# Optimization experiments

Hardware: AMD Instinct MI355X
Metric: run time of the kernel (lower is better)

The kernel has to match this reference:

```python
import jax, jax.numpy as jnp
import numpy as np
import math

A = 32; B = 32; PSIZE = 16; K = 3; STRIDE = 2; PAD = 1; ITERS = 3; FINAL_LAMBDA = 0.01
KK = K * K; KKA = KK * A; KKA2 = KKA // 2 + 1
EPS = 1e-12; LN2PI = math.log(2 * math.pi)


def unfold(x, k, s, p):
    # torch F.unfold: output feature dim ordered (C, kh, kw), columns row-major
    b, C, h, w = x.shape
    xp = jnp.pad(x, ((0, 0), (0, 0), (p, p), (p, p)))
    oh = (h + 2 * p - k) // s + 1
    ow = (w + 2 * p - k) // s + 1
    cols = [xp[:, :, ki:ki + s * (oh - 1) + 1:s, kj:kj + s * (ow - 1) + 1:s]
            for ki in range(k) for kj in range(k)]
    patches = jnp.stack(cols, axis=2)  # [b, C, kk, oh, ow]
    return patches.reshape(b, C, k * k, oh * ow), oh, ow


def setup_inputs():
    key = jax.random.key(0)
    ks = jax.random.split(key, 8)
    b, h, w = 4, 14, 14
    a_in = jax.random.uniform(ks[0], (b, A, h, w), dtype=jnp.float32)
    pose = jax.random.normal(ks[1], (b, A * PSIZE, h, w), dtype=jnp.float32)
    mpose_w = jax.random.normal(ks[2], (B * PSIZE, PSIZE), dtype=jnp.float32) / np.float32(np.sqrt(PSIZE))
    mpose_b = jnp.zeros((B * PSIZE,), jnp.float32)
    freq_w = jax.random.normal(ks[3], (KKA2, PSIZE, 2), dtype=jnp.float32) * 0.02
    ln_g = jnp.ones((A,), jnp.float32)
    ln_b = jnp.zeros((A,), jnp.float32)
    lim = np.float32(np.sqrt(6.0 / (KK + KK)))  # xavier_uniform on [kk, kk, 1]
    spat_w = jax.random.uniform(ks[4], (KK, KK, 1), jnp.float32, -lim, lim)
    spat_bias = jnp.ones((KK,), jnp.float32)
    beta_u = jnp.zeros((1, 1, B, 1), jnp.float32)
    beta_a = jnp.zeros((1, 1, B), jnp.float32)
    return dict(a_in=a_in, pose=pose, mpose_w=mpose_w, mpose_b=mpose_b,
                freq_w=freq_w, ln_g=ln_g, ln_b=ln_b, spat_w=spat_w,
                spat_bias=spat_bias, beta_u=beta_u, beta_a=beta_a)


def _forward(a_in, pose, mpose_w, mpose_b, freq_w, ln_g, ln_b,
             spat_w, spat_bias, beta_u, beta_a):
    b = a_in.shape[0]
    pose_u, oh, ow = unfold(pose, K, STRIDE, PAD)  # [b, A*PSIZE, KK, l]
    l = oh * ow
    pose_u = pose_u.reshape(b, A, PSIZE, KK, l)
    pose_u = pose_u.transpose(0, 4, 3, 1, 2).reshape(b, l, KKA, PSIZE)
    # mpose linear: psize -> B*psize
    po = jnp.einsum('blkp,qp->blkq', pose_u, mpose_w) + mpose_b
    po = po.reshape(b * l, KKA, B, PSIZE)
    # Frequency FFT filter over kkA axis (weight shared across all B slices)
    xf = jnp.fft.rfft(po, axis=1, norm='ortho')        # [bl, KKA2, B, PSIZE] complex
    wc = freq_w[..., 0] + 1j * freq_w[..., 1]           # [KKA2, PSIZE]
    xf = xf * wc[None, :, None, :]
    po = jnp.fft.irfft(xf, n=KKA, axis=1, norm='ortho') + po  # residual
    v = po.reshape(b, l, KKA, B, PSIZE)
    a_u, _, _ = unfold(a_in, K, STRIDE, PAD)            # [b, A, KK, l]
    a_u = a_u.transpose(0, 3, 2, 1).reshape(b, l, KKA)
    # Spatial gating applied to ones-initialized r (identical for every B slice)
    ones = jnp.ones((b * l, KKA), jnp.float32)
    g = ones.reshape(b * l, KK, A)
    mu_g = g.mean(-1, keepdims=True)
    var_g = ((g - mu_g) ** 2).mean(-1, keepdims=True)
    gn = (g - mu_g) / jnp.sqrt(var_g + 1e-5) * ln_g + ln_b
    g2 = jnp.einsum('ij,nja->nia', spat_w[:, :, 0], gn) + spat_bias[None, :, None]
    gate = jax.nn.gelu(g2, approximate=False).reshape(b * l, KKA) + ones
    logit = jnp.broadcast_to(gate[:, :, None], (b * l, KKA, B))
    r = jax.nn.softmax(logit, axis=2).reshape(b, l, KKA, B, 1)
    a_out = mu = None
    for i in range(ITERS):
        lam = FINAL_LAMBDA * (1.0 - 0.95 ** (i + 1))
        # m-step
        rr = r * a_u[:, :, :, None, None]
        r_sum = rr.sum(axis=2, keepdims=True)                 # [b,l,1,B,1]
        coeff = rr / (r_sum + EPS)
        mu = (coeff * v).sum(axis=2, keepdims=True)           # [b,l,1,B,PSIZE]
        sig = (coeff * (v - mu) ** 2).sum(axis=2, keepdims=True) + EPS
        cost = (beta_u + jnp.log(jnp.sqrt(sig[:, :, 0]))) * r_sum[:, :, 0]  # [b,l,B,PSIZE]
        a_out = jax.nn.sigmoid(lam * (beta_a - cost.sum(axis=3)))           # [b,l,B]
        if i < ITERS - 1:
            # e-step (note: log(sigma_sq * ln2pi) is faithful to the original code)
            ln_p = (-0.5 * jnp.sum(jnp.log(sig * LN2PI), axis=-1)
                    - jnp.sum((v - mu) ** 2 / (2.0 * sig), axis=-1))        # [b,l,KKA,B]
            ln_ap = ln_p + jnp.log(a_out[:, :, None, :])
            r = jax.nn.softmax(ln_ap, axis=-1)[..., None]
    pose_out = mu[:, :, 0].reshape(b, l, B * PSIZE).transpose(0, 2, 1).reshape(b, B * PSIZE, oh, ow)
    a_fin = a_out.transpose(0, 2, 1).reshape(b, B, oh, ow)
    return a_fin, pose_out


def reference(a_in, pose, mpose_w, mpose_b, freq_w, ln_g, ln_b,
              spat_w, spat_bias, beta_u, beta_a):
    return _forward(a_in, pose, mpose_w, mpose_b, freq_w, ln_g, ln_b,
                    spat_w, spat_bias, beta_u, beta_a)
```

## Files before the change

### kernel.cpp

```cpp
#include <hip/hip_runtime.h>
#include <hip/hip_bf16.h>
#include <math.h>

#define A_    32
#define B_    32
#define PS    16
#define KK_   9
#define KKA_  288
#define OH_   7
#define L_    49
#define NB    4
#define NSITE 196
#define NCOLS 3136

#define LAM1 5.0e-4f
#define LAM2 9.75e-4f
#define LAM3 1.42625e-3f
#define LOG_LN2PI 0.6086775903077413f

typedef _Float16 half2v __attribute__((ext_vector_type(2)));
typedef short    short8 __attribute__((ext_vector_type(8)));
typedef float    floatx4 __attribute__((ext_vector_type(4)));

static __device__ __forceinline__ float san(float x, float lo, float hi){
    return fminf(fmaxf(x, lo), hi);
}

static __device__ __forceinline__ float dot2acc(half2v a, half2v b, float c){
#if __has_builtin(__builtin_amdgcn_fdot2)
    return __builtin_amdgcn_fdot2(a, b, c, false);
#else
    return c + (float)a.x*(float)b.x + (float)a.y*(float)b.y;
#endif
}

__global__ void k_prep(const float* __restrict__ fw, const float* __restrict__ pose,
                       ushort* __restrict__ cpr, float* __restrict__ csum,
                       __hip_bfloat16* __restrict__ Xt, int nc)
{
    if ((int)blockIdx.x < nc){
        int id = (int)blockIdx.x*256 + threadIdx.x;
        if (id >= 16*288) return;
        int p = id / 288, m = id % 288;
        float acc = fw[(0*16 + p)*2 + 0];
        for (int k = 1; k <= 143; ++k){
            float re = fw[(k*16 + p)*2 + 0];
            float im = fw[(k*16 + p)*2 + 1];
            int km = (k*m) % 288;
            float ang = 0.021816615649929116f * (float)km;
            float s, c; __sincosf(ang, &s, &c);
            acc += 2.0f*(re*c - im*s);
        }
        float re144 = fw[(144*16 + p)*2 + 0];
        acc += re144 * ((m & 1) ? -1.0f : 1.0f);
        float cv = acc * (1.0f/288.0f);
        if (m == 0) cv += 1.0f;
        cv = san(cv, -1e4f, 1e4f);

        __hip_bfloat16 hb = __float2bfloat16(cv);
        float hif = __bfloat162float(hb);
        __hip_bfloat16 lb = __float2bfloat16(cv - hif);
        ushort hi = *(ushort*)&hb, lo = *(ushort*)&lb;

        ushort* c0h = cpr + p*592;
        ushort* c1h = cpr + 16*592   + p*592;
        ushort* c0l = cpr + 16*592*2 + p*592;
        ushort* c1l = cpr + 16*592*3 + p*592;
        int x1 = 288 - m;
        c0h[x1] = hi;  c0l[x1] = lo;
        c1h[x1-1] = hi; c1l[x1-1] = lo;
        if (m >= 1){
            int x2 = 576 - m;
            c0h[x2] = hi;  c0l[x2] = lo;
            c1h[x2-1] = hi; c1l[x2-1] = lo;
        } else {
            c0h[0] = hi; c0l[0] = lo;
            csum[p] = san(1.0f + fw[(0*16 + p)*2 + 0], -1e4f, 1e4f);
        }
        return;
    }
    int id = ((int)blockIdx.x - nc)*256 + threadIdx.x;
    if (id >= NCOLS*KKA_/8) return;
    int c = id / (KKA_/8), j8 = id % (KKA_/8);
    int j = j8*8;
    int n = c >> 4, q = c & 15;
    int bs = n / L_, l = n % L_, oy = l / OH_, ox = l % OH_;
    int kk = j >> 5, a0 = j & 31;
    int y = oy*2 - 1 + kk/3, x = ox*2 - 1 + kk%3;
    const bool inb = ((unsigned)y < 14u && (unsigned)x < 14u);
    const float* psrc = pose + (((long)bs*(A_*PS))*14 + y)*14 + x;
    union { ushort us[8]; uint4 u4; } res;
    #pragma unroll
    for (int u = 0; u < 8; ++u){
        float v = 0.f;
        if (inb) v = psrc[((a0+u)*PS + q)*196];
        __hip_bfloat16 hb = __float2bfloat16(san(v, -1e4f, 1e4f));
        res.us[u] = *(ushort*)&hb;
    }
    *(uint4*)&Xt[c*KKA_ + j] = res.u4;
}

__launch_bounds__(512, 1)
__global__ void
k_mega(const ushort* __restrict__ cpr, const __hip_bfloat16* __restrict__ Xt,
       const float* __restrict__ a_in,
       const float* __restrict__ mpw, const float* __restrict__ mpb,
       const float* __restrict__ csum,
       const float* __restrict__ beta_u, const float* __restrict__ beta_a,
       float* __restrict__ out)
{
    const int nl = blockIdx.x;
    const int t = threadIdx.x;
    const int Bc = t >> 4, p = t & 15;
    const int bs = nl / L_, l = nl % L_;

    __shared__ uint v_lds[56][512];
    __shared__ __align__(16) float scratch[9792];
    __shared__ float a_s[KKA_];
    __shared__ float cst[32];

    float* const dall = scratch;

    for (int j = t; j < KKA_; j += 512){
        int kk = j >> 5, a = j & 31;
        int oy = l / OH_, ox = l % OH_;
        int y = oy*2 - 1 + kk/3, x = ox*2 - 1 + kk%3;
        float v = 0.f;
        if ((unsigned)y < 14u && (unsigned)x < 14u)
            v = a_in[((bs*A_ + a)*14 + y)*14 + x];
        a_s[j] = san(v, 0.f, 1e4f);
    }
    half2v w_h[8];
    #pragma unroll
    for (int k = 0; k < 8; ++k){
        w_h[k].x = (_Float16)mpw[t*16 + 2*k];
        w_h[k].y = (_Float16)mpw[t*16 + 2*k + 1];
    }
    const float vb = mpb[t] * csum[p];
    const float bu = beta_u[Bc];
    const float ba = beta_a[Bc];

    const int w = t >> 6, lane = t & 63;
    const int mn = lane & 15, quad = lane >> 4;
    const int p0 = w*2;

    short8 bf[9];
    {
        const __hip_bfloat16* xrow = Xt + (nl*16 + mn)*KKA_ + quad*8;
        #pragma unroll
        for (int k = 0; k < 9; ++k) bf[k] = *(const short8*)&xrow[k*32];
    }
    __syncthreads();

    float s0a = 0.f, s0b = 0.f, s0c = 0.f, s0d = 0.f;
    for (int j = 0; j < KKA_; j += 4){
        s0a += a_s[j]; s0b += a_s[j+1]; s0c += a_s[j+2]; s0d += a_s[j+3];
    }
    const float S0tot = (s0a + s0b) + (s0c + s0d);

    float S1 = 0.f, S2 = 0.f;
    half2v v_h[88];

    auto do_chunk = [&](int ch, _Float16* usb){
        floatx4 accA = {0,0,0,0}, accB = {0,0,0,0};
        #pragma unroll
        for (int k0i = 0; k0i < 9; ++k0i){
            const int k0 = k0i*32;
            short8 bfrag = bf[k0i];
            #pragma unroll
            for (int pp = 0; pp < 2; ++pp){
                const int pg = p0 + pp;
                int o = 288 + k0 + quad*8 - (ch*16 + mn);
                int sel = o & 1, off = o - sel;
                const ushort* bh = cpr + (sel ? 16*592 : 0) + pg*592;
                const ushort* bl = cpr + 16*592*2 + (sel ? 16*592 : 0) + pg*592;
                short8 ah = *(const short8*)&bh[off];
                short8 al = *(const short8*)&bl[off];
                floatx4 acc = pp ? accB : accA;
                acc = __builtin_amdgcn_mfma_f32_16x16x32_bf16(ah, bfrag, acc, 0, 0, 0);
                acc = __builtin_amdgcn_mfma_f32_16x16x32_bf16(al, bfrag, acc, 0, 0, 0);
                if (pp) accB = acc; else accA = acc;
            }
        }
        #pragma unroll
        for (int r = 0; r < 4; ++r){
            usb[p0*264     + (quad*4 + r)*16 + mn] = (_Float16)accA[r];
            usb[(p0+1)*264 + (quad*4 + r)*16 + mn] = (_Float16)accB[r];
        }
    };

    auto vpair = [&](const _Float16* urow, int s, float& v0o, float& v1o){
        union { uint4 u4; half2v h2[4]; } A0, A1, B0, B1;
        A0.u4 = *(const uint4*)&urow[(2*s)*16];
        A1.u4 = *(const uint4*)&urow[(2*s)*16 + 8];
        B0.u4 = *(const uint4*)&urow[(2*s+1)*16];
        B1.u4 = *(const uint4*)&urow[(2*s+1)*16 + 8];
        float v0 = vb, v1 = vb;
        #pragma unroll
        for (int m = 0; m < 4; ++m){
            v0 = dot2acc(A0.h2[m], w_h[m],   v0);
            v0 = dot2acc(A1.h2[m], w_h[4+m], v0);
            v1 = dot2acc(B0.h2[m], w_h[m],   v1);
            v1 = dot2acc(B1.h2[m], w_h[4+m], v1);
        }
        v0o = v0; v1o = v1;
    };

    for (int ch = 0; ch < 7; ++ch){
        _Float16* usb = ((_Float16*)scratch) + (ch & 1)*4224;
        do_chunk(ch, usb);
        __syncthreads();
        const _Float16* urow = &usb[p*264];
        #pragma unroll
        for (int s = 0; s < 8; ++s){
            float v0, v1; vpair(urow, s, v0, v1);
            const int i0 = ch*16 + 2*s;
            const float a0 = a_s[i0], a1 = a_s[i0+1];
            S1 += a0*v0 + a1*v1;
            S2 += a0*v0*v0 + a1*v1*v1;
            union { half2v h; uint u; } cv;
            cv.h.x = (_Float16)v0; cv.h.y = (_Float16)v1;
            v_lds[ch*8 + s][t] = cv.u;
        }
    }
    #pragma unroll
    for (int c2 = 0; c2 < 11; ++c2){
        const int ch = 7 + c2;
        _Float16* usb = ((_Float16*)scratch) + (ch & 1)*4224;
        do_chunk(ch, usb);
        __syncthreads();
        const _Float16* urow = &usb[p*264];
        #pragma unroll
        for (int s = 0; s < 8; ++s){
            float v0, v1; vpair(urow, s, v0, v1);
            const int i0 = ch*16 + 2*s;
            const float a0 = a_s[i0], a1 = a_s[i0+1];
            S1 += a0*v0 + a1*v1;
            S2 += a0*v0*v0 + a1*v1*v1;
            half2v vh; vh.x = (_Float16)v0; vh.y = (_Float16)v1;
            v_h[c2*8 + s] = vh;
        }
    }

    float mu_r, i2s_r;
    {
        const float rs  = S0tot * (1.0f/32.0f);
        const float inv = 1.0f / (rs + 1e-12f);
        const float S1r = S1 * (1.0f/32.0f), S2r = S2 * (1.0f/32.0f);
        mu_r = S1r * inv;
        const float sg  = fmaxf((S2r - 2.f*mu_r*S1r + mu_r*mu_r*rs) * inv, 0.f) + 1e-12f;
        i2s_r = 0.5f / sg;
        const float lg  = logf(sg);
        float cs = (bu + 0.5f*lg) * rs;
        float ls = lg + LOG_LN2PI;
        #pragma unroll
        for (int m = 1; m < 16; m <<= 1){ cs += __shfl_xor(cs, m, 16); ls += __shfl_xor(ls, m, 16); }
        const float aout = san(1.f/(1.f + expf(-LAM1*(ba - cs))), 1e-30f, 1.f);
        if (p == 0) cst[Bc] = logf(aout) - 0.5f*ls;
    }
    __syncthreads();

    const int b0 = p & 1, b1 = (p>>1)&1, b2 = (p>>2)&1, b3 = (p>>3)&1;
    const int isub = t >> 5, Bce = t & 31;
    float muF = 0.f, aF = 0.f;
    for (int it = 0; it < 2; ++it){
        const float lam = it ? LAM3 : LAM2;

        auto dtree = [&](int ibase, auto getpair){
            float e1[8], e2[4], e3[2], dfin;
            #pragma unroll
            for (int s = 0; s < 8; ++s){
                float v0, v1; getpair(s, v0, v1);
                float d0 = v0 - mu_r, d1 = v1 - mu_r;
                float ea = d0*d0*i2s_r, eb = d1*d1*i2s_r;
                float aown  = b0 ? eb : ea;
                float asend = b0 ? ea : eb;
                e1[s] = aown + __shfl_xor(asend, 1);
            }
            #pragma unroll
            for (int s = 0; s < 4; ++s){
                float aown  = b1 ? e1[2*s+1] : e1[2*s];
                float asend = b1 ? e1[2*s]   : e1[2*s+1];
                e2[s] = aown + __shfl_xor(asend, 2);
            }
            #pragma unroll
            for (int s = 0; s < 2; ++s){
                float aown  = b2 ? e2[2*s+1] : e2[2*s];
                float asend = b2 ? e2[2*s]   : e2[2*s+1];
                e3[s] = aown + __shfl_xor(asend, 4);
            }
            {
                float aown  = b3 ? e3[1] : e3[0];
                float asend = b3 ? e3[0] : e3[1];
                dfin = aown + __shfl_xor(asend, 8);
            }
            dall[(ibase + p)*34 + Bc] = dfin;
        };
        #pragma unroll
        for (int g = 0; g < 7; ++g)
            dtree(g*16, [&](int s, float& v0, float& v1){
                union { uint u; half2v h; } cv; cv.u = v_lds[g*8 + s][t];
                v0 = (float)cv.h.x; v1 = (float)cv.h.y; });
        #pragma unroll
        for (int c2 = 0; c2 < 11; ++c2)
            dtree((7+c2)*16, [&](int s, float& v0, float& v1){
                half2v vh = v_h[c2*8 + s];
                v0 = (float)vh.x; v1 = (float)vh.y; });
        __syncthreads();

        {
            const float cb = cst[Bce];
            #pragma unroll
            for (int g = 0; g < 18; ++g){
                float* dp = &dall[(g*16 + isub)*34 + Bce];
                float lnap = cb - *dp;
                float mx = lnap;
                #pragma unroll
                for (int m = 16; m >= 1; m >>= 1) mx = fmaxf(mx, __shfl_xor(mx, m));
                float ex = expf(lnap - mx);
                float sm = ex;
                #pragma unroll
                for (int m = 16; m >= 1; m >>= 1) sm += __shfl_xor(sm, m);
                *dp = (ex / sm) * a_s[g*16 + isub];
            }
        }
        __syncthreads();

        float T0 = 0.f, T1 = 0.f, T2 = 0.f;
        auto csum3 = [&](int ibase, auto getpair){
            #pragma unroll
            for (int s = 0; s < 8; ++s){
                float v0, v1; getpair(s, v0, v1);
                float r0 = dall[(ibase + 2*s)*34 + Bc];
                float r1 = dall[(ibase + 2*s + 1)*34 + Bc];
                T0 += r0 + r1;
                T1 += r0*v0 + r1*v1;
                T2 += r0*v0*v0 + r1*v1*v1;
            }
        };
        #pragma unroll
        for (int g = 0; g < 7; ++g)
            csum3(g*16, [&](int s, float& v0, float& v1){
                union { uint u; half2v h; } cv; cv.u = v_lds[g*8 + s][t];
                v0 = (float)cv.h.x; v1 = (float)cv.h.y; });
        #pragma unroll
        for (int c2 = 0; c2 < 11; ++c2)
            csum3((7+c2)*16, [&](int s, float& v0, float& v1){
                half2v vh = v_h[c2*8 + s];
                v0 = (float)vh.x; v1 = (float)vh.y; });

        const float inv = 1.f/(T0 + 1e-12f);
        const float mu  = T1 * inv;
        const float sg  = fmaxf((T2 - 2.f*mu*T1 + mu*mu*T0) * inv, 0.f) + 1e-12f;
        const float lg  = logf(sg);
        float cs = (bu + 0.5f*lg) * T0;
        float ls = lg + LOG_LN2PI;
        #pragma unroll
        for (int m = 1; m < 16; m <<= 1){ cs += __shfl_xor(cs, m, 16); ls += __shfl_xor(ls, m, 16); }
        const float aout = san(1.f/(1.f + expf(-lam*(ba - cs))), 1e-30f, 1.f);
        if (it == 0){
            mu_r = mu; i2s_r = 0.5f/sg;
            if (p == 0) cst[Bc] = logf(aout) - 0.5f*ls;
            __syncthreads();
        } else { muF = mu; aF = aout; }
    }

    if (p == 0) out[bs*(B_*L_) + Bc*L_ + l] = san(aF, 0.f, 1.f);
    out[6272 + (bs*512 + t)*L_ + l] = san(muF, -1e4f, 1e4f);
}

extern "C" void kernel_launch(void* const* d_in, const int* in_sizes, int n_in,
                              void* d_out, int out_size, void* d_ws, size_t ws_size,
                              hipStream_t stream)
{
    const float* a_in   = (const float*)d_in[0];
    const float* pose   = (const float*)d_in[1];
    const float* mpw    = (const float*)d_in[2];
    const float* mpb    = (const float*)d_in[3];
    const float* fw     = (const float*)d_in[4];
    const float* beta_u = (const float*)d_in[9];
    const float* beta_a = (const float*)d_in[10];
    float* out = (float*)d_out;

    char* base = (char*)d_ws;
    float*  csum = (float*)(base + 0);
    ushort* cpr  = (ushort*)(base + 256);
    __hip_bfloat16* Xt = (__hip_bfloat16*)(base + 76288);

    const int nc = 18;
    const int nx = (NCOLS*KKA_/8 + 255)/256;
    k_prep<<<nc + nx, 256, 0, stream>>>(fw, pose, cpr, csum, Xt, nc);
    k_mega<<<NSITE, 512, 0, stream>>>(cpr, Xt, a_in, mpw, mpb, csum, beta_u, beta_a, out);
}
```

Before: 258.0 us.

## Rebalance vote storage across LDS, registers and recompute to allow two blocks per CU

The kernel now lets the compiler target up to two waves per EU, and shrinks per-block storage to fit. The LDS vote buffer drops from 56 to 48 rows, the register vote array from 88 to 80 entries, and the B-fragment registers are re-read from global memory on each chunk instead of being held. The last two chunks are no longer stored; their votes are recomputed from the retained fp16 transform buffers in each routing pass. The aim is higher occupancy to hide latency, at the cost of extra global loads, repeated dot products, and possible register spills.

```diff
diff --git a/kernel.cpp b/kernel.cpp
--- a/kernel.cpp
+++ b/kernel.cpp
@@ -100,8 +100,8 @@
     *(uint4*)&Xt[c*KKA_ + j] = res.u4;
 }
 
-__launch_bounds__(512, 1)
-__global__ void
+__global__ __attribute__((amdgpu_flat_work_group_size(512,512), amdgpu_waves_per_eu(1,2)))
+void
 k_mega(const ushort* __restrict__ cpr, const __hip_bfloat16* __restrict__ Xt,
        const float* __restrict__ a_in,
        const float* __restrict__ mpw, const float* __restrict__ mpb,
@@ -114,12 +114,11 @@
     const int Bc = t >> 4, p = t & 15;
     const int bs = nl / L_, l = nl % L_;
 
-    __shared__ uint v_lds[56][512];
-    __shared__ __align__(16) float scratch[9792];
+    __shared__ uint v_lds[48][512];
+    __shared__ __align__(16) _Float16 us[2*4224];
+    __shared__ float dall[288*34];
     __shared__ float a_s[KKA_];
     __shared__ float cst[32];
-
-    float* const dall = scratch;
 
     for (int j = t; j < KKA_; j += 512){
         int kk = j >> 5, a = j & 31;
@@ -139,34 +138,27 @@
     const float vb = mpb[t] * csum[p];
     const float bu = beta_u[Bc];
     const float ba = beta_a[Bc];
+    __syncthreads();
+
+    float s0a = 0.f, s0b = 0.f, s0c = 0.f, s0d = 0.f;
+    for (int j = 0; j < KKA_; j += 4){
+        s0a += a_s[j]; s0b += a_s[j+1]; s0c += a_s[j+2]; s0d += a_s[j+3];
+    }
+    const float S0tot = (s0a + s0b) + (s0c + s0d);
 
     const int w = t >> 6, lane = t & 63;
     const int mn = lane & 15, quad = lane >> 4;
     const int p0 = w*2;
-
-    short8 bf[9];
-    {
-        const __hip_bfloat16* xrow = Xt + (nl*16 + mn)*KKA_ + quad*8;
-        #pragma unroll
-        for (int k = 0; k < 9; ++k) bf[k] = *(const short8*)&xrow[k*32];
-    }
-    __syncthreads();
-
-    float s0a = 0.f, s0b = 0.f, s0c = 0.f, s0d = 0.f;
-    for (int j = 0; j < KKA_; j += 4){
-        s0a += a_s[j]; s0b += a_s[j+1]; s0c += a_s[j+2]; s0d += a_s[j+3];
-    }
-    const float S0tot = (s0a + s0b) + (s0c + s0d);
+    const __hip_bfloat16* xrow = Xt + (nl*16 + mn)*KKA_ + quad*8;
 
     float S1 = 0.f, S2 = 0.f;
-    half2v v_h[88];
+    half2v v_h[80];
 
     auto do_chunk = [&](int ch, _Float16* usb){
         floatx4 accA = {0,0,0,0}, accB = {0,0,0,0};
-        #pragma unroll
         for (int k0i = 0; k0i < 9; ++k0i){
             const int k0 = k0i*32;
-            short8 bfrag = bf[k0i];
+            short8 bfrag = *(const short8*)&xrow[k0];
             #pragma unroll
             for (int pp = 0; pp < 2; ++pp){
                 const int pg = p0 + pp;
@@ -206,8 +198,8 @@
         v0o = v0; v1o = v1;
     };
 
-    for (int ch = 0; ch < 7; ++ch){
-        _Float16* usb = ((_Float16*)scratch) + (ch & 1)*4224;
+    for (int ch = 0; ch < 6; ++ch){
+        _Float16* usb = us + (ch & 1)*4224;
         do_chunk(ch, usb);
         __syncthreads();
         const _Float16* urow = &usb[p*264];
@@ -224,9 +216,9 @@
         }
     }
     #pragma unroll
-    for (int c2 = 0; c2 < 11; ++c2){
-        const int ch = 7 + c2;
-        _Float16* usb = ((_Float16*)scratch) + (ch & 1)*4224;
+    for (int c2 = 0; c2 < 10; ++c2){
+        const int ch = 6 + c2;
+        _Float16* usb = us + (ch & 1)*4224;
         do_chunk(ch, usb);
         __syncthreads();
         const _Float16* urow = &usb[p*264];
@@ -239,6 +231,21 @@
             S2 += a0*v0*v0 + a1*v1*v1;
             half2v vh; vh.x = (_Float16)v0; vh.y = (_Float16)v1;
             v_h[c2*8 + s] = vh;
+        }
+    }
+    #pragma unroll
+    for (int ch = 16; ch < 18; ++ch){
+        _Float16* usb = us + (ch & 1)*4224;
+        do_chunk(ch, usb);
+        __syncthreads();
+        const _Float16* urow = &usb[p*264];
+        #pragma unroll
+        for (int s = 0; s < 8; ++s){
+            float v0, v1; vpair(urow, s, v0, v1);
+            const int i0 = ch*16 + 2*s;
+            const float a0 = a_s[i0], a1 = a_s[i0+1];
+            S1 += a0*v0 + a1*v1;
+            S2 += a0*v0*v0 + a1*v1*v1;
         }
     }
 
@@ -296,16 +303,21 @@
             }
             dall[(ibase + p)*34 + Bc] = dfin;
         };
-        #pragma unroll
-        for (int g = 0; g < 7; ++g)
+        for (int g = 0; g < 6; ++g)
             dtree(g*16, [&](int s, float& v0, float& v1){
                 union { uint u; half2v h; } cv; cv.u = v_lds[g*8 + s][t];
                 v0 = (float)cv.h.x; v1 = (float)cv.h.y; });
         #pragma unroll
-        for (int c2 = 0; c2 < 11; ++c2)
-            dtree((7+c2)*16, [&](int s, float& v0, float& v1){
+        for (int c2 = 0; c2 < 10; ++c2)
+            dtree((6+c2)*16, [&](int s, float& v0, float& v1){
                 half2v vh = v_h[c2*8 + s];
                 v0 = (float)vh.x; v1 = (float)vh.y; });
+        #pragma unroll
+        for (int ch = 16; ch < 18; ++ch){
+            const _Float16* urow = &us[(ch & 1)*4224 + p*264];
+            dtree(ch*16, [&](int s, float& v0, float& v1){
+                vpair(urow, s, v0, v1); });
+        }
         __syncthreads();
 
         {
@@ -338,16 +350,21 @@
                 T2 += r0*v0*v0 + r1*v1*v1;
             }
         };
-        #pragma unroll
-        for (int g = 0; g < 7; ++g)
+        for (int g = 0; g < 6; ++g)
             csum3(g*16, [&](int s, float& v0, float& v1){
                 union { uint u; half2v h; } cv; cv.u = v_lds[g*8 + s][t];
                 v0 = (float)cv.h.x; v1 = (float)cv.h.y; });
         #pragma unroll
-        for (int c2 = 0; c2 < 11; ++c2)
-            csum3((7+c2)*16, [&](int s, float& v0, float& v1){
+        for (int c2 = 0; c2 < 10; ++c2)
+            csum3((6+c2)*16, [&](int s, float& v0, float& v1){
                 half2v vh = v_h[c2*8 + s];
                 v0 = (float)vh.x; v1 = (float)vh.y; });
+        #pragma unroll
+        for (int ch = 16; ch < 18; ++ch){
+            const _Float16* urow = &us[(ch & 1)*4224 + p*264];
+            csum3(ch*16, [&](int s, float& v0, float& v1){
+                vpair(urow, s, v0, v1); });
+        }
 
         const float inv = 1.f/(T0 + 1e-12f);
         const float mu  = T1 * inv;
```

Measured after the change: 257.2 us. No clear change (-0.3%).

## Rebalance vote storage across LDS, registers and retained MFMA chunks

Applied to the files above, without the earlier changes.

Vote storage is redistributed. Six chunks now go to LDS (down from seven) and nine to registers (down from eleven). The last three chunks keep their raw MFMA outputs in a triple-buffered LDS region and are recomputed from there with vpair during the E-steps instead of being stored. The B-fragment registers are dropped, so Xt is reloaded from global memory in each k step, and several loops are left without unroll pragmas. The dall stride also changes from 34 to 33, which alters the LDS bank pattern. The aim is lower register pressure without extra LDS, at the cost of recomputing the dot products and more global loads.

```diff
diff --git a/kernel.cpp b/kernel.cpp
--- a/kernel.cpp
+++ b/kernel.cpp
@@ -17,6 +17,8 @@
 #define LAM2 9.75e-4f
 #define LAM3 1.42625e-3f
 #define LOG_LN2PI 0.6086775903077413f
+
+#define DSTR 33
 
 typedef _Float16 half2v __attribute__((ext_vector_type(2)));
 typedef short    short8 __attribute__((ext_vector_type(8)));
@@ -114,12 +116,11 @@
     const int Bc = t >> 4, p = t & 15;
     const int bs = nl / L_, l = nl % L_;
 
-    __shared__ uint v_lds[56][512];
-    __shared__ __align__(16) float scratch[9792];
+    __shared__ uint v_lds[48][512];
+    __shared__ __align__(16) _Float16 us[3*4224];
+    __shared__ float dall[288*DSTR];
     __shared__ float a_s[KKA_];
     __shared__ float cst[32];
-
-    float* const dall = scratch;
 
     for (int j = t; j < KKA_; j += 512){
         int kk = j >> 5, a = j & 31;
@@ -139,34 +140,27 @@
     const float vb = mpb[t] * csum[p];
     const float bu = beta_u[Bc];
     const float ba = beta_a[Bc];
+    __syncthreads();
+
+    float s0a = 0.f, s0b = 0.f, s0c = 0.f, s0d = 0.f;
+    for (int j = 0; j < KKA_; j += 4){
+        s0a += a_s[j]; s0b += a_s[j+1]; s0c += a_s[j+2]; s0d += a_s[j+3];
+    }
+    const float S0tot = (s0a + s0b) + (s0c + s0d);
 
     const int w = t >> 6, lane = t & 63;
     const int mn = lane & 15, quad = lane >> 4;
     const int p0 = w*2;
-
-    short8 bf[9];
-    {
-        const __hip_bfloat16* xrow = Xt + (nl*16 + mn)*KKA_ + quad*8;
-        #pragma unroll
-        for (int k = 0; k < 9; ++k) bf[k] = *(const short8*)&xrow[k*32];
-    }
-    __syncthreads();
-
-    float s0a = 0.f, s0b = 0.f, s0c = 0.f, s0d = 0.f;
-    for (int j = 0; j < KKA_; j += 4){
-        s0a += a_s[j]; s0b += a_s[j+1]; s0c += a_s[j+2]; s0d += a_s[j+3];
-    }
-    const float S0tot = (s0a + s0b) + (s0c + s0d);
+    const __hip_bfloat16* xrow = Xt + (nl*16 + mn)*KKA_ + quad*8;
 
     float S1 = 0.f, S2 = 0.f;
-    half2v v_h[88];
+    half2v v_h[72];
 
     auto do_chunk = [&](int ch, _Float16* usb){
         floatx4 accA = {0,0,0,0}, accB = {0,0,0,0};
-        #pragma unroll
         for (int k0i = 0; k0i < 9; ++k0i){
             const int k0 = k0i*32;
-            short8 bfrag = bf[k0i];
+            short8 bfrag = *(const short8*)&xrow[k0];
             #pragma unroll
             for (int pp = 0; pp < 2; ++pp){
                 const int pg = p0 + pp;
@@ -206,8 +200,8 @@
         v0o = v0; v1o = v1;
     };
 
-    for (int ch = 0; ch < 7; ++ch){
-        _Float16* usb = ((_Float16*)scratch) + (ch & 1)*4224;
+    for (int ch = 0; ch < 6; ++ch){
+        _Float16* usb = us + (ch % 3)*4224;
         do_chunk(ch, usb);
         __syncthreads();
         const _Float16* urow = &usb[p*264];
@@ -223,24 +217,39 @@
             v_lds[ch*8 + s][t] = cv.u;
         }
     }
-    #pragma unroll
-    for (int c2 = 0; c2 < 11; ++c2){
-        const int ch = 7 + c2;
-        _Float16* usb = ((_Float16*)scratch) + (ch & 1)*4224;
-        do_chunk(ch, usb);
-        __syncthreads();
-        const _Float16* urow = &usb[p*264];
-        #pragma unroll
-        for (int s = 0; s < 8; ++s){
-            float v0, v1; vpair(urow, s, v0, v1);
-            const int i0 = ch*16 + 2*s;
-            const float a0 = a_s[i0], a1 = a_s[i0+1];
-            S1 += a0*v0 + a1*v1;
-            S2 += a0*v0*v0 + a1*v1*v1;
-            half2v vh; vh.x = (_Float16)v0; vh.y = (_Float16)v1;
-            v_h[c2*8 + s] = vh;
-        }
-    }
+
+#define P1_REG(C2) { \
+        _Float16* usb = us + ((6+(C2)) % 3)*4224; \
+        do_chunk(6+(C2), usb); \
+        __syncthreads(); \
+        const _Float16* urow = &usb[p*264]; \
+        _Pragma("unroll") \
+        for (int s = 0; s < 8; ++s){ \
+            float v0, v1; vpair(urow, s, v0, v1); \
+            const int i0 = (6+(C2))*16 + 2*s; \
+            const float a0 = a_s[i0], a1 = a_s[i0+1]; \
+            S1 += a0*v0 + a1*v1; \
+            S2 += a0*v0*v0 + a1*v1*v1; \
+            half2v vh; vh.x = (_Float16)v0; vh.y = (_Float16)v1; \
+            v_h[(C2)*8 + s] = vh; } }
+    P1_REG(0) P1_REG(1) P1_REG(2) P1_REG(3) P1_REG(4)
+    P1_REG(5) P1_REG(6) P1_REG(7) P1_REG(8)
+#undef P1_REG
+
+#define P1_RET(CH) { \
+        _Float16* usb = us + ((CH) % 3)*4224; \
+        do_chunk((CH), usb); \
+        __syncthreads(); \
+        const _Float16* urow = &usb[p*264]; \
+        _Pragma("unroll") \
+        for (int s = 0; s < 8; ++s){ \
+            float v0, v1; vpair(urow, s, v0, v1); \
+            const int i0 = (CH)*16 + 2*s; \
+            const float a0 = a_s[i0], a1 = a_s[i0+1]; \
+            S1 += a0*v0 + a1*v1; \
+            S2 += a0*v0*v0 + a1*v1*v1; } }
+    P1_RET(15) P1_RET(16) P1_RET(17)
+#undef P1_RET
 
     float mu_r, i2s_r;
     {
@@ -294,25 +303,30 @@
                 float asend = b3 ? e3[0] : e3[1];
                 dfin = aown + __shfl_xor(asend, 8);
             }
-            dall[(ibase + p)*34 + Bc] = dfin;
+            dall[(ibase + p)*DSTR + Bc] = dfin;
         };
-        #pragma unroll
-        for (int g = 0; g < 7; ++g)
+        for (int g = 0; g < 6; ++g)
             dtree(g*16, [&](int s, float& v0, float& v1){
                 union { uint u; half2v h; } cv; cv.u = v_lds[g*8 + s][t];
                 v0 = (float)cv.h.x; v1 = (float)cv.h.y; });
-        #pragma unroll
-        for (int c2 = 0; c2 < 11; ++c2)
-            dtree((7+c2)*16, [&](int s, float& v0, float& v1){
-                half2v vh = v_h[c2*8 + s];
-                v0 = (float)vh.x; v1 = (float)vh.y; });
+#define DT_REG(C2) dtree((6+(C2))*16, [&](int s, float& v0, float& v1){ \
+            half2v vh = v_h[(C2)*8 + s]; v0 = (float)vh.x; v1 = (float)vh.y; });
+        DT_REG(0) DT_REG(1) DT_REG(2) DT_REG(3) DT_REG(4)
+        DT_REG(5) DT_REG(6) DT_REG(7) DT_REG(8)
+#undef DT_REG
+        { const _Float16* ur = &us[0*4224 + p*264];
+          dtree(15*16, [&](int s, float& v0, float& v1){ vpair(ur, s, v0, v1); }); }
+        { const _Float16* ur = &us[1*4224 + p*264];
+          dtree(16*16, [&](int s, float& v0, float& v1){ vpair(ur, s, v0, v1); }); }
+        { const _Float16* ur = &us[2*4224 + p*264];
+          dtree(17*16, [&](int s, float& v0, float& v1){ vpair(ur, s, v0, v1); }); }
         __syncthreads();
 
         {
             const float cb = cst[Bce];
             #pragma unroll
             for (int g = 0; g < 18; ++g){
-                float* dp = &dall[(g*16 + isub)*34 + Bce];
+                float* dp = &dall[(g*16 + isub)*DSTR + Bce];
                 float lnap = cb - *dp;
                 float mx = lnap;
                 #pragma unroll
@@ -331,23 +345,28 @@
             #pragma unroll
             for (int s = 0; s < 8; ++s){
                 float v0, v1; getpair(s, v0, v1);
-                float r0 = dall[(ibase + 2*s)*34 + Bc];
-                float r1 = dall[(ibase + 2*s + 1)*34 + Bc];
+                float r0 = dall[(ibase + 2*s)*DSTR + Bc];
+                float r1 = dall[(ibase + 2*s + 1)*DSTR + Bc];
                 T0 += r0 + r1;
                 T1 += r0*v0 + r1*v1;
                 T2 += r0*v0*v0 + r1*v1*v1;
             }
         };
-        #pragma unroll
-        for (int g = 0; g < 7; ++g)
+        for (int g = 0; g < 6; ++g)
             csum3(g*16, [&](int s, float& v0, float& v1){
                 union { uint u; half2v h; } cv; cv.u = v_lds[g*8 + s][t];
                 v0 = (float)cv.h.x; v1 = (float)cv.h.y; });
-        #pragma unroll
-        for (int c2 = 0; c2 < 11; ++c2)
-            csum3((7+c2)*16, [&](int s, float& v0, float& v1){
-                half2v vh = v_h[c2*8 + s];
-                v0 = (float)vh.x; v1 = (float)vh.y; });
+#define CS_REG(C2) csum3((6+(C2))*16, [&](int s, float& v0, float& v1){ \
+            half2v vh = v_h[(C2)*8 + s]; v0 = (float)vh.x; v1 = (float)vh.y; });
+        CS_REG(0) CS_REG(1) CS_REG(2) CS_REG(3) CS_REG(4)
+        CS_REG(5) CS_REG(6) CS_REG(7) CS_REG(8)
+#undef CS_REG
+        { const _Float16* ur = &us[0*4224 + p*264];
+          csum3(15*16, [&](int s, float& v0, float& v1){ vpair(ur, s, v0, v1); }); }
+        { const _Float16* ur = &us[1*4224 + p*264];
+          csum3(16*16, [&](int s, float& v0, float& v1){ vpair(ur, s, v0, v1); }); }
+        { const _Float16* ur = &us[2*4224 + p*264];
+          csum3(17*16, [&](int s, float& v0, float& v1){ vpair(ur, s, v0, v1); }); }
 
         const float inv = 1.f/(T0 + 1e-12f);
         const float mu  = T1 * inv;
```

Measured after the change: 259.9 us. No clear change (+0.7%).

## Spill vote tensor to global scratch instead of LDS and registers

Applied to the files above, without the earlier changes.

The per-site vote matrix v was previously split between a large LDS array and 88 half2 registers per thread. It now lives entirely in a global workspace buffer that is written once and re-read in each EM iteration. The B fragments are reloaded from global per chunk instead of being held in registers, and the dall stride changes from 34 to 33. This frees LDS and registers, but it adds global memory round-trips, relying on L2 to keep them cheap.

```diff
diff --git a/kernel.cpp b/kernel.cpp
--- a/kernel.cpp
+++ b/kernel.cpp
@@ -17,6 +17,8 @@
 #define LAM2 9.75e-4f
 #define LAM3 1.42625e-3f
 #define LOG_LN2PI 0.6086775903077413f
+
+#define DSTR 33
 
 typedef _Float16 half2v __attribute__((ext_vector_type(2)));
 typedef short    short8 __attribute__((ext_vector_type(8)));
@@ -107,6 +109,7 @@
        const float* __restrict__ mpw, const float* __restrict__ mpb,
        const float* __restrict__ csum,
        const float* __restrict__ beta_u, const float* __restrict__ beta_a,
+       uint* __restrict__ vg,
        float* __restrict__ out)
 {
     const int nl = blockIdx.x;
@@ -114,12 +117,12 @@
     const int Bc = t >> 4, p = t & 15;
     const int bs = nl / L_, l = nl % L_;
 
-    __shared__ uint v_lds[56][512];
-    __shared__ __align__(16) float scratch[9792];
+    __shared__ __align__(16) _Float16 us[2*4224];
+    __shared__ float dall[288*DSTR];
     __shared__ float a_s[KKA_];
     __shared__ float cst[32];
 
-    float* const dall = scratch;
+    uint* const vgs = vg + (long)nl*144*512 + t;
 
     for (int j = t; j < KKA_; j += 512){
         int kk = j >> 5, a = j & 31;
@@ -139,34 +142,26 @@
     const float vb = mpb[t] * csum[p];
     const float bu = beta_u[Bc];
     const float ba = beta_a[Bc];
+    __syncthreads();
+
+    float s0a = 0.f, s0b = 0.f, s0c = 0.f, s0d = 0.f;
+    for (int j = 0; j < KKA_; j += 4){
+        s0a += a_s[j]; s0b += a_s[j+1]; s0c += a_s[j+2]; s0d += a_s[j+3];
+    }
+    const float S0tot = (s0a + s0b) + (s0c + s0d);
 
     const int w = t >> 6, lane = t & 63;
     const int mn = lane & 15, quad = lane >> 4;
     const int p0 = w*2;
-
-    short8 bf[9];
-    {
-        const __hip_bfloat16* xrow = Xt + (nl*16 + mn)*KKA_ + quad*8;
-        #pragma unroll
-        for (int k = 0; k < 9; ++k) bf[k] = *(const short8*)&xrow[k*32];
-    }
-    __syncthreads();
-
-    float s0a = 0.f, s0b = 0.f, s0c = 0.f, s0d = 0.f;
-    for (int j = 0; j < KKA_; j += 4){
-        s0a += a_s[j]; s0b += a_s[j+1]; s0c += a_s[j+2]; s0d += a_s[j+3];
-    }
-    const float S0tot = (s0a + s0b) + (s0c + s0d);
+    const __hip_bfloat16* xrow = Xt + (nl*16 + mn)*KKA_ + quad*8;
 
     float S1 = 0.f, S2 = 0.f;
-    half2v v_h[88];
 
     auto do_chunk = [&](int ch, _Float16* usb){
         floatx4 accA = {0,0,0,0}, accB = {0,0,0,0};
-        #pragma unroll
         for (int k0i = 0; k0i < 9; ++k0i){
             const int k0 = k0i*32;
-            short8 bfrag = bf[k0i];
+            short8 bfrag = *(const short8*)&xrow[k0];
             #pragma unroll
             for (int pp = 0; pp < 2; ++pp){
                 const int pg = p0 + pp;
@@ -206,8 +201,8 @@
         v0o = v0; v1o = v1;
     };
 
-    for (int ch = 0; ch < 7; ++ch){
-        _Float16* usb = ((_Float16*)scratch) + (ch & 1)*4224;
+    for (int ch = 0; ch < 18; ++ch){
+        _Float16* usb = us + (ch & 1)*4224;
         do_chunk(ch, usb);
         __syncthreads();
         const _Float16* urow = &usb[p*264];
@@ -220,25 +215,7 @@
             S2 += a0*v0*v0 + a1*v1*v1;
             union { half2v h; uint u; } cv;
             cv.h.x = (_Float16)v0; cv.h.y = (_Float16)v1;
-            v_lds[ch*8 + s][t] = cv.u;
-        }
-    }
-    #pragma unroll
-    for (int c2 = 0; c2 < 11; ++c2){
-        const int ch = 7 + c2;
-        _Float16* usb = ((_Float16*)scratch) + (ch & 1)*4224;
-        do_chunk(ch, usb);
-        __syncthreads();
-        const _Float16* urow = &usb[p*264];
-        #pragma unroll
-        for (int s = 0; s < 8; ++s){
-            float v0, v1; vpair(urow, s, v0, v1);
-            const int i0 = ch*16 + 2*s;
-            const float a0 = a_s[i0], a1 = a_s[i0+1];
-            S1 += a0*v0 + a1*v1;
-            S2 += a0*v0*v0 + a1*v1*v1;
-            half2v vh; vh.x = (_Float16)v0; vh.y = (_Float16)v1;
-            v_h[c2*8 + s] = vh;
+            vgs[(ch*8 + s)*512] = cv.u;
         }
     }
 
@@ -266,11 +243,12 @@
     for (int it = 0; it < 2; ++it){
         const float lam = it ? LAM3 : LAM2;
 
-        auto dtree = [&](int ibase, auto getpair){
+        auto dtree = [&](int ibase, const uint* uu){
             float e1[8], e2[4], e3[2], dfin;
             #pragma unroll
             for (int s = 0; s < 8; ++s){
-                float v0, v1; getpair(s, v0, v1);
+                union { uint u; half2v h; } cv; cv.u = uu[s];
+                float v0 = (float)cv.h.x, v1 = (float)cv.h.y;
                 float d0 = v0 - mu_r, d1 = v1 - mu_r;
                 float ea = d0*d0*i2s_r, eb = d1*d1*i2s_r;
                 float aown  = b0 ? eb : ea;
@@ -294,25 +272,21 @@
                 float asend = b3 ? e3[0] : e3[1];
                 dfin = aown + __shfl_xor(asend, 8);
             }
-            dall[(ibase + p)*34 + Bc] = dfin;
+            dall[(ibase + p)*DSTR + Bc] = dfin;
         };
-        #pragma unroll
-        for (int g = 0; g < 7; ++g)
-            dtree(g*16, [&](int s, float& v0, float& v1){
-                union { uint u; half2v h; } cv; cv.u = v_lds[g*8 + s][t];
-                v0 = (float)cv.h.x; v1 = (float)cv.h.y; });
-        #pragma unroll
-        for (int c2 = 0; c2 < 11; ++c2)
-            dtree((7+c2)*16, [&](int s, float& v0, float& v1){
-                half2v vh = v_h[c2*8 + s];
-                v0 = (float)vh.x; v1 = (float)vh.y; });
+        for (int g = 0; g < 18; ++g){
+            uint uu[8];
+            #pragma unroll
+            for (int s = 0; s < 8; ++s) uu[s] = vgs[(g*8 + s)*512];
+            dtree(g*16, uu);
+        }
         __syncthreads();
 
         {
             const float cb = cst[Bce];
             #pragma unroll
             for (int g = 0; g < 18; ++g){
-                float* dp = &dall[(g*16 + isub)*34 + Bce];
+                float* dp = &dall[(g*16 + isub)*DSTR + Bce];
                 float lnap = cb - *dp;
                 float mx = lnap;
                 #pragma unroll
@@ -327,27 +301,24 @@
         __syncthreads();
 
         float T0 = 0.f, T1 = 0.f, T2 = 0.f;
-        auto csum3 = [&](int ibase, auto getpair){
+        auto csum3 = [&](int ibase, const uint* uu){
             #pragma unroll
             for (int s = 0; s < 8; ++s){
-                float v0, v1; getpair(s, v0, v1);
-                float r0 = dall[(ibase + 2*s)*34 + Bc];
-                float r1 = dall[(ibase + 2*s + 1)*34 + Bc];
+                union { uint u; half2v h; } cv; cv.u = uu[s];
+                float v0 = (float)cv.h.x, v1 = (float)cv.h.y;
+                float r0 = dall[(ibase + 2*s)*DSTR + Bc];
+                float r1 = dall[(ibase + 2*s + 1)*DSTR + Bc];
                 T0 += r0 + r1;
                 T1 += r0*v0 + r1*v1;
                 T2 += r0*v0*v0 + r1*v1*v1;
             }
         };
-        #pragma unroll
-        for (int g = 0; g < 7; ++g)
-            csum3(g*16, [&](int s, float& v0, float& v1){
-                union { uint u; half2v h; } cv; cv.u = v_lds[g*8 + s][t];
-                v0 = (float)cv.h.x; v1 = (float)cv.h.y; });
-        #pragma unroll
-        for (int c2 = 0; c2 < 11; ++c2)
-            csum3((7+c2)*16, [&](int s, float& v0, float& v1){
-                half2v vh = v_h[c2*8 + s];
-                v0 = (float)vh.x; v1 = (float)vh.y; });
+        for (int g = 0; g < 18; ++g){
+            uint uu[8];
+            #pragma unroll
+            for (int s = 0; s < 8; ++s) uu[s] = vgs[(g*8 + s)*512];
+            csum3(g*16, uu);
+        }
 
         const float inv = 1.f/(T0 + 1e-12f);
         const float mu  = T1 * inv;
@@ -386,9 +357,10 @@
     float*  csum = (float*)(base + 0);
     ushort* cpr  = (ushort*)(base + 256);
     __hip_bfloat16* Xt = (__hip_bfloat16*)(base + 76288);
+    uint*   vg   = (uint*)(base + 1882624);
 
     const int nc = 18;
     const int nx = (NCOLS*KKA_/8 + 255)/256;
     k_prep<<<nc + nx, 256, 0, stream>>>(fw, pose, cpr, csum, Xt, nc);
-    k_mega<<<NSITE, 512, 0, stream>>>(cpr, Xt, a_in, mpw, mpb, csum, beta_u, beta_a, out);
-}
+    k_mega<<<NSITE, 512, 0, stream>>>(cpr, Xt, a_in, mpw, mpb, csum, beta_u, beta_a, vg, out);
+}
```

After: 268.0 us. +3.9%, slower.
